# Performance work log

Hardware: AMD Instinct MI355X
Metric: run time of the kernel (lower is better)

Reference implementation:

```python
import jax, jax.numpy as jnp
import numpy as np

B = 8192
IN = 2048   # input_size
H = 2048    # hidden_size
D = IN + H  # combine feature dim = 4096


def setup_inputs() -> dict:
    key = jax.random.key(0)
    ks = jax.random.split(key, 11)
    s = 1.0 / np.sqrt(D)  # nn.Linear default init scale
    inp = {
        "input": jax.random.normal(ks[0], (B, D), jnp.float32),
        "hidden": jax.random.normal(ks[1], (B, D), jnp.float32),
        "cell": jax.random.normal(ks[2], (B, H), jnp.float32),
        "Wf": jax.random.uniform(ks[3], (D, H), jnp.float32, -s, s),
        "bf": jax.random.uniform(ks[4], (H,), jnp.float32, -s, s),
        "Wc": jax.random.uniform(ks[5], (D, H), jnp.float32, -s, s),
        "bc": jax.random.uniform(ks[6], (H,), jnp.float32, -s, s),
        "Wi": jax.random.uniform(ks[7], (D, H), jnp.float32, -s, s),
        "bi": jax.random.uniform(ks[8], (H,), jnp.float32, -s, s),
        "Wo": jax.random.uniform(ks[9], (D, H), jnp.float32, -s, s),
        "bo": jax.random.uniform(ks[10], (H,), jnp.float32, -s, s),
    }
    return inp


def reference(input, hidden, cell, Wf, bf, Wc, bc, Wi, bi, Wo, bo):
    combine = input + hidden  # [B, D] elementwise add (as in source, not concat)
    # Fuse the 4 gate GEMMs into one [D, 4H] GEMM for efficiency (same math).
    W = jnp.concatenate([Wf, Wc, Wi, Wo], axis=1)  # [D, 4H]
    b = jnp.concatenate([bf, bc, bi, bo])          # [4H]
    gates = combine @ W + b                        # [B, 4H]
    gf, gc, gi, go = jnp.split(gates, 4, axis=1)
    ft = jax.nn.sigmoid(gf)
    ct_ = jnp.tanh(gc)
    it = jax.nn.sigmoid(jax.nn.sigmoid(gi))  # double sigmoid, faithful to source
    cell_state = cell * ft + ct_ * it
    out = jax.nn.sigmoid(go)
    hidden_state = out * jnp.tanh(cell_state)
    return (out, hidden_state, cell_state)
```

## Files before the change

### kernel.cpp

```cpp
#include <hip/hip_runtime.h>
#include <hip/hip_bf16.h>

#define B_SZ 8192
#define D_SZ 4096
#define H_SZ 2048
#define N4H  8192
#define NT   (D_SZ / 64)

typedef __attribute__((ext_vector_type(8))) __bf16 bf16x8;
typedef __attribute__((ext_vector_type(4))) float f32x4;

#define GPTR(p) ((__attribute__((address_space(1))) void*)(p))
#define LPTR(p) ((__attribute__((address_space(3))) void*)(p))

__global__ void prep_k(const float* __restrict__ x, const float* __restrict__ h,
                       __hip_bfloat16* __restrict__ comb,
                       const float* __restrict__ Wf, const float* __restrict__ Wc,
                       const float* __restrict__ Wi, const float* __restrict__ Wo,
                       __hip_bfloat16* __restrict__ WT) {
    __shared__ float t[32][33];
    if (blockIdx.x < 2048) {
        const size_t n4 = (size_t)B_SZ * D_SZ / 4;
        const size_t stride = (size_t)2048 * 256;
        for (size_t i = (size_t)blockIdx.x * 256 + threadIdx.x; i < n4; i += stride) {
            f32x4 a = __builtin_nontemporal_load((const f32x4*)x + i);
            f32x4 b = __builtin_nontemporal_load((const f32x4*)h + i);
            short4 r;
            r.x = __builtin_bit_cast(short, __float2bfloat16(a.x + b.x));
            r.y = __builtin_bit_cast(short, __float2bfloat16(a.y + b.y));
            r.z = __builtin_bit_cast(short, __float2bfloat16(a.z + b.z));
            r.w = __builtin_bit_cast(short, __float2bfloat16(a.w + b.w));
            ((short4*)comb)[i] = r;
        }
    } else {
        const int b = blockIdx.x - 2048;
        const int k0 = (b & 127) * 32;
        const int n0 = (b >> 7) * 32;
        const float* W = (n0 < H_SZ) ? Wf : (n0 < 2 * H_SZ) ? Wc
                       : (n0 < 3 * H_SZ) ? Wi : Wo;
        const int g = n0 >> 11;
        const int nc = n0 & (H_SZ - 1);
        const int tx = threadIdx.x & 31, ty = threadIdx.x >> 5;
#pragma unroll
        for (int j = 0; j < 4; ++j)
            t[ty + j * 8][tx] = __builtin_nontemporal_load(
                W + (size_t)(k0 + ty + j * 8) * H_SZ + nc + tx);
        __syncthreads();
#pragma unroll
        for (int j = 0; j < 4; ++j) {
            const int h2 = nc + ty + j * 8;
            const int np = ((h2 >> 4) << 6) + (g << 4) + (h2 & 15);
            WT[(size_t)np * D_SZ + k0 + tx] = __float2bfloat16(t[tx][ty + j * 8]);
        }
    }
}


#define BAR()                                    \
    do {                                         \
        asm volatile("" ::: "memory");           \
        __builtin_amdgcn_s_barrier();            \
        asm volatile("" ::: "memory");           \
    } while (0)

#define STAGE(pbase, HSTRIDE, h, kt, region)                                           \
    do {                                                                               \
        __builtin_amdgcn_global_load_lds(                                              \
            GPTR((pbase) + (size_t)((h) * (HSTRIDE)) * D_SZ + (size_t)(kt) * 64),      \
            LPTR(smem + (region) + (h) * 16384 + wave * 1024), 16, 0, 0);              \
        __builtin_amdgcn_global_load_lds(                                              \
            GPTR((pbase) + (size_t)(128 + (h) * (HSTRIDE)) * D_SZ + (size_t)(kt) * 64),\
            LPTR(smem + (region) + (h) * 16384 + 8192 + wave * 1024), 16, 0, 0);       \
    } while (0)

#define LDA(dst, base, qm)                                                             \
    do {                                                                               \
        _Pragma("unroll") for (int mi = 0; mi < 4; ++mi) {                             \
            const int row_ = (qm) * 128 + wr * 64 + mi * 16 + fr;                      \
            dst[mi][0] = *(const bf16x8*)(smem + (base) + row_ * 128 + sw0);           \
            dst[mi][1] = *(const bf16x8*)(smem + (base) + row_ * 128 + sw1);           \
        }                                                                              \
    } while (0)

#define LDB(dst, base, qn)                                                             \
    do {                                                                               \
        _Pragma("unroll") for (int nf = 0; nf < 2; ++nf) {                             \
            const int row_ = (qn) * 128 + wc * 32 + nf * 16 + fr;                      \
            dst[nf][0] = *(const bf16x8*)(smem + (base) + row_ * 128 + sw0);           \
            dst[nf][1] = *(const bf16x8*)(smem + (base) + row_ * 128 + sw1);           \
        }                                                                              \
    } while (0)

#define MFMA_Q(qm, qn, areg, breg)                                                     \
    do {                                                                               \
        _Pragma("unroll") for (int mi = 0; mi < 4; ++mi)                               \
        _Pragma("unroll") for (int nf = 0; nf < 2; ++nf)                               \
        _Pragma("unroll") for (int ks = 0; ks < 2; ++ks)                               \
            acc[(qm) * 4 + mi][(qn) * 2 + nf] =                                        \
                __builtin_amdgcn_mfma_f32_16x16x32_bf16(                               \
                    areg[mi][ks], breg[nf][ks],                                        \
                    acc[(qm) * 4 + mi][(qn) * 2 + nf], 0, 0, 0);                       \
    } while (0)

#define TILE(tcur, CA, CB, OB)                                                         \
    {                                                                                  \
                                                                  \
        LDA(a, CA, 0);                                                                 \
        LDB(b0, CB, 0);                                                                \
        if ((tcur) + 1 < NT) STAGE(pB, 32, 1, (tcur) + 1, OB);                         \
        BAR();                                                                         \
        asm volatile("s_waitcnt lgkmcnt(0)" ::: "memory");                             \
        __builtin_amdgcn_s_setprio(1);                                                 \
        MFMA_Q(0, 0, a, b0);                                                           \
        __builtin_amdgcn_s_setprio(0);                                                 \
        BAR();                                                                         \
                                                                  \
        LDB(b1, CB, 1);                                                                \
        if ((tcur) + 2 < NT) STAGE(pA, 64, 0, (tcur) + 2, CA);                         \
        BAR();                                                                         \
        asm volatile("s_waitcnt lgkmcnt(0)" ::: "memory");                             \
        __builtin_amdgcn_s_setprio(1);                                                 \
        MFMA_Q(0, 1, a, b1);                                                           \
        __builtin_amdgcn_s_setprio(0);                                                 \
        BAR();                                                                         \
                                                                  \
        LDA(a, CA, 1);                                                                 \
        if ((tcur) + 2 < NT) STAGE(pB, 32, 0, (tcur) + 2, CB);                         \
        BAR();                                                                         \
        asm volatile("s_waitcnt lgkmcnt(0)" ::: "memory");                             \
        __builtin_amdgcn_s_setprio(1);                                                 \
        MFMA_Q(1, 0, a, b0);                                                           \
        __builtin_amdgcn_s_setprio(0);                                                 \
        BAR();                                                                         \
                                                                  \
        if ((tcur) + 2 < NT) STAGE(pA, 64, 1, (tcur) + 2, CA);                         \
        BAR();                                                                         \
        __builtin_amdgcn_s_setprio(1);                                                 \
        MFMA_Q(1, 1, a, b1);                                                           \
        __builtin_amdgcn_s_setprio(0);                                                 \
        if ((tcur) + 2 < NT) {                                                         \
            asm volatile("s_waitcnt vmcnt(6)" ::: "memory");                           \
        } else if ((tcur) + 1 < NT) {                                                  \
            asm volatile("s_waitcnt vmcnt(0)" ::: "memory");                           \
        }                                                                              \
        BAR();                                                                         \
    }

__device__ __forceinline__ float fsig(float x) { return 1.f / (1.f + __expf(-x)); }
__device__ __forceinline__ float ftanh(float x) {
    x = fminf(fmaxf(x, -15.f), 15.f);
    float e = __expf(2.f * x);
    return (e - 1.f) / (e + 1.f);
}

__global__ __launch_bounds__(512, 2) void gemm8_k(
    const __hip_bfloat16* __restrict__ A,
    const __hip_bfloat16* __restrict__ BT,
    const float* __restrict__ cell,
    const float* __restrict__ bfb, const float* __restrict__ bcb,
    const float* __restrict__ bib, const float* __restrict__ bob,
    float* __restrict__ out)
{
    extern __shared__ char smem[];

    const int tid  = threadIdx.x;
    const int wave = tid >> 6;
    const int lane = tid & 63;
    const int wr = wave >> 2;
    const int wc = wave & 3;
    const int fr = lane & 15;
    const int sw0 = (((lane >> 4) + 0) ^ (fr & 7)) << 4;
    const int sw1 = (((lane >> 4) + 4) ^ (fr & 7)) << 4;

    const int wg = (blockIdx.x & 7) * 128 + (blockIdx.x >> 3);
    const int n0 = (wg & 31) * 256;
    const int m0 = (wg >> 5) * 256;

    const int r0   = tid >> 3;
    const int col0 = ((tid & 7) ^ (r0 & 7)) << 3;
    const __hip_bfloat16* pA = A  + (size_t)(m0 + r0) * D_SZ + col0;
    const __hip_bfloat16* pB = BT + (size_t)(n0 + ((r0 >> 5) << 6) + (r0 & 31)) * D_SZ + col0;

    f32x4 acc[8][4] = {};
    bf16x8 a[4][2], b0[2][2], b1[2][2];

    STAGE(pA, 64, 0, 0, 0);
    STAGE(pB, 32, 0, 0, 32768);
    STAGE(pA, 64, 1, 0, 0);
    STAGE(pB, 32, 1, 0, 32768);
    STAGE(pA, 64, 0, 1, 65536);
    STAGE(pB, 32, 0, 1, 98304);
    STAGE(pA, 64, 1, 1, 65536);
    asm volatile("s_waitcnt vmcnt(6)" ::: "memory");
    BAR();

    for (int t = 0; t < NT; t += 2) {
        TILE(t,     0,     32768, 98304);
        TILE(t + 1, 65536, 98304, 32768);
    }

    const int crow = (lane >> 4) * 4;
    const int ccol = lane & 15;
    const int hh = (((n0 + wc * 64) >> 6) << 4) + ccol;
    const float bf_ = bfb[hh], bc_ = bcb[hh], bi_ = bib[hh], bo_ = bob[hh];
    const size_t BH = (size_t)B_SZ * H_SZ;
    float* hidp = out + BH;
    float* cstp = out + 2 * BH;
#pragma unroll
    for (int ai = 0; ai < 8; ++ai) {
#pragma unroll
        for (int j = 0; j < 4; ++j) {
            const size_t r = (size_t)(m0 + wr * 128 + ai * 16 + crow + j);
            const size_t idx = r * H_SZ + hh;
            const float gf = acc[ai][0][j] + bf_;
            const float gc = acc[ai][1][j] + bc_;
            const float gi = acc[ai][2][j] + bi_;
            const float go = acc[ai][3][j] + bo_;
            const float ft = fsig(gf);
            const float ct = ftanh(gc);
            const float it = fsig(fsig(gi));
            const float ot = fsig(go);
            const float cv = __builtin_nontemporal_load(cell + idx);
            const float cs = cv * ft + ct * it;
            __builtin_nontemporal_store(ot, out + idx);
            __builtin_nontemporal_store(cs, cstp + idx);
            __builtin_nontemporal_store(ot * ftanh(cs), hidp + idx);
        }
    }
}

extern "C" void kernel_launch(void* const* d_in, const int* in_sizes, int n_in,
                              void* d_out, int out_size, void* d_ws, size_t ws_size,
                              hipStream_t stream) {
    const float* input  = (const float*)d_in[0];
    const float* hidden = (const float*)d_in[1];
    const float* cell   = (const float*)d_in[2];
    const float* Wf     = (const float*)d_in[3];
    const float* bfb    = (const float*)d_in[4];
    const float* Wc     = (const float*)d_in[5];
    const float* bcb    = (const float*)d_in[6];
    const float* Wi     = (const float*)d_in[7];
    const float* bib    = (const float*)d_in[8];
    const float* Wo     = (const float*)d_in[9];
    const float* bob    = (const float*)d_in[10];
    float* out = (float*)d_out;

    char* ws = (char*)d_ws;
    __hip_bfloat16* comb = (__hip_bfloat16*)ws;
    __hip_bfloat16* WT   = (__hip_bfloat16*)(ws + (size_t)B_SZ * D_SZ * 2);

    hipFuncSetAttribute(reinterpret_cast<const void*>(gemm8_k),
                        hipFuncAttributeMaxDynamicSharedMemorySize, 131072);

    prep_k<<<2048 + 32768, 256, 0, stream>>>(input, hidden, comb, Wf, Wc, Wi, Wo, WT);
    gemm8_k<<<1024, 512, 131072, stream>>>(comb, WT, cell, bfb, bcb, bib, bob, out);
}
```

Before: 630.6 us.

## Make GEMM persistent: each block iterates four M tiles with cross-tile prefetch

The GEMM launch shrinks from 1024 to 256 blocks. Each block now owns one N column strip and loops over four consecutive 256-row M tiles on its XCD. While the current tile finishes, the first K tiles of the next M tile are prefetched into the pipeline, so the prologue and epilogue bubbles between tiles are hidden and the B strip stays hot in cache. In exchange, 256 blocks with 2 per CU give one wave of work with no tail balancing, and the epilogue stores now sit inside the main loop.

```diff
diff --git a/kernel.cpp b/kernel.cpp
--- a/kernel.cpp
+++ b/kernel.cpp
@@ -102,9 +102,44 @@
                     acc[(qm) * 4 + mi][(qn) * 2 + nf], 0, 0, 0);                       \
     } while (0)
 
-#define TILE(tcur, CA, CB, OB)                                                         \
+#define TILE_FULL(CA, CB, OB, PA2, K1, K2)                                             \
     {                                                                                  \
-                                                                  \
+        LDA(a, CA, 0);                                                                 \
+        LDB(b0, CB, 0);                                                                \
+        STAGE(pB, 32, 1, (K1), OB);                                                    \
+        BAR();                                                                         \
+        asm volatile("s_waitcnt lgkmcnt(0)" ::: "memory");                             \
+        __builtin_amdgcn_s_setprio(1);                                                 \
+        MFMA_Q(0, 0, a, b0);                                                           \
+        __builtin_amdgcn_s_setprio(0);                                                 \
+        BAR();                                                                         \
+        LDB(b1, CB, 1);                                                                \
+        STAGE(PA2, 64, 0, (K2), CA);                                                   \
+        BAR();                                                                         \
+        asm volatile("s_waitcnt lgkmcnt(0)" ::: "memory");                             \
+        __builtin_amdgcn_s_setprio(1);                                                 \
+        MFMA_Q(0, 1, a, b1);                                                           \
+        __builtin_amdgcn_s_setprio(0);                                                 \
+        BAR();                                                                         \
+        LDA(a, CA, 1);                                                                 \
+        STAGE(pB, 32, 0, (K2), CB);                                                    \
+        BAR();                                                                         \
+        asm volatile("s_waitcnt lgkmcnt(0)" ::: "memory");                             \
+        __builtin_amdgcn_s_setprio(1);                                                 \
+        MFMA_Q(1, 0, a, b0);                                                           \
+        __builtin_amdgcn_s_setprio(0);                                                 \
+        BAR();                                                                         \
+        STAGE(PA2, 64, 1, (K2), CA);                                                   \
+        BAR();                                                                         \
+        __builtin_amdgcn_s_setprio(1);                                                 \
+        MFMA_Q(1, 1, a, b1);                                                           \
+        __builtin_amdgcn_s_setprio(0);                                                 \
+        asm volatile("s_waitcnt vmcnt(6)" ::: "memory");                               \
+        BAR();                                                                         \
+    }
+
+#define TILE_TAIL(tcur, CA, CB, OB)                                                    \
+    {                                                                                  \
         LDA(a, CA, 0);                                                                 \
         LDB(b0, CB, 0);                                                                \
         if ((tcur) + 1 < NT) STAGE(pB, 32, 1, (tcur) + 1, OB);                         \
@@ -114,33 +149,25 @@
         MFMA_Q(0, 0, a, b0);                                                           \
         __builtin_amdgcn_s_setprio(0);                                                 \
         BAR();                                                                         \
-                                                                  \
         LDB(b1, CB, 1);                                                                \
-        if ((tcur) + 2 < NT) STAGE(pA, 64, 0, (tcur) + 2, CA);                         \
         BAR();                                                                         \
         asm volatile("s_waitcnt lgkmcnt(0)" ::: "memory");                             \
         __builtin_amdgcn_s_setprio(1);                                                 \
         MFMA_Q(0, 1, a, b1);                                                           \
         __builtin_amdgcn_s_setprio(0);                                                 \
         BAR();                                                                         \
-                                                                  \
         LDA(a, CA, 1);                                                                 \
-        if ((tcur) + 2 < NT) STAGE(pB, 32, 0, (tcur) + 2, CB);                         \
         BAR();                                                                         \
         asm volatile("s_waitcnt lgkmcnt(0)" ::: "memory");                             \
         __builtin_amdgcn_s_setprio(1);                                                 \
         MFMA_Q(1, 0, a, b0);                                                           \
         __builtin_amdgcn_s_setprio(0);                                                 \
         BAR();                                                                         \
-                                                                  \
-        if ((tcur) + 2 < NT) STAGE(pA, 64, 1, (tcur) + 2, CA);                         \
         BAR();                                                                         \
         __builtin_amdgcn_s_setprio(1);                                                 \
         MFMA_Q(1, 1, a, b1);                                                           \
         __builtin_amdgcn_s_setprio(0);                                                 \
-        if ((tcur) + 2 < NT) {                                                         \
-            asm volatile("s_waitcnt vmcnt(6)" ::: "memory");                           \
-        } else if ((tcur) + 1 < NT) {                                                  \
+        if ((tcur) + 1 < NT) {                                                         \
             asm volatile("s_waitcnt vmcnt(0)" ::: "memory");                           \
         }                                                                              \
         BAR();                                                                         \
@@ -172,14 +199,26 @@
     const int sw0 = (((lane >> 4) + 0) ^ (fr & 7)) << 4;
     const int sw1 = (((lane >> 4) + 4) ^ (fr & 7)) << 4;
 
-    const int wg = (blockIdx.x & 7) * 128 + (blockIdx.x >> 3);
-    const int n0 = (wg & 31) * 256;
-    const int m0 = (wg >> 5) * 256;
+    const int xcd  = blockIdx.x & 7;
+    const int slot = blockIdx.x >> 3;
+    const int n0 = slot * 256;
 
     const int r0   = tid >> 3;
     const int col0 = ((tid & 7) ^ (r0 & 7)) << 3;
-    const __hip_bfloat16* pA = A  + (size_t)(m0 + r0) * D_SZ + col0;
-    const __hip_bfloat16* pB = BT + (size_t)(n0 + ((r0 >> 5) << 6) + (r0 & 31)) * D_SZ + col0;
+    const __hip_bfloat16* pB =
+        BT + (size_t)(n0 + ((r0 >> 5) << 6) + (r0 & 31)) * D_SZ + col0;
+
+    const __hip_bfloat16* pA =
+        A + (size_t)(xcd * 1024 + r0) * D_SZ + col0;
+    const __hip_bfloat16* pA_nx = pA + (size_t)256 * D_SZ;
+
+    const int crow = (lane >> 4) * 4;
+    const int ccol = lane & 15;
+    const int hh = (slot * 4 + wc) * 16 + ccol;
+    const float bf_ = bfb[hh], bc_ = bcb[hh], bi_ = bib[hh], bo_ = bob[hh];
+    const size_t BH = (size_t)B_SZ * H_SZ;
+    float* hidp = out + BH;
+    float* cstp = out + 2 * BH;
 
     f32x4 acc[8][4] = {};
     bf16x8 a[4][2], b0[2][2], b1[2][2];
@@ -194,38 +233,52 @@
     asm volatile("s_waitcnt vmcnt(6)" ::: "memory");
     BAR();
 
-    for (int t = 0; t < NT; t += 2) {
-        TILE(t,     0,     32768, 98304);
-        TILE(t + 1, 65536, 98304, 32768);
-    }
-
-    const int crow = (lane >> 4) * 4;
-    const int ccol = lane & 15;
-    const int hh = (((n0 + wc * 64) >> 6) << 4) + ccol;
-    const float bf_ = bfb[hh], bc_ = bcb[hh], bi_ = bib[hh], bo_ = bob[hh];
-    const size_t BH = (size_t)B_SZ * H_SZ;
-    float* hidp = out + BH;
-    float* cstp = out + 2 * BH;
-#pragma unroll
-    for (int ai = 0; ai < 8; ++ai) {
-#pragma unroll
-        for (int j = 0; j < 4; ++j) {
-            const size_t r = (size_t)(m0 + wr * 128 + ai * 16 + crow + j);
-            const size_t idx = r * H_SZ + hh;
-            const float gf = acc[ai][0][j] + bf_;
-            const float gc = acc[ai][1][j] + bc_;
-            const float gi = acc[ai][2][j] + bi_;
-            const float go = acc[ai][3][j] + bo_;
-            const float ft = fsig(gf);
-            const float ct = ftanh(gc);
-            const float it = fsig(fsig(gi));
-            const float ot = fsig(go);
-            const float cv = __builtin_nontemporal_load(cell + idx);
-            const float cs = cv * ft + ct * it;
-            __builtin_nontemporal_store(ot, out + idx);
-            __builtin_nontemporal_store(cs, cstp + idx);
-            __builtin_nontemporal_store(ot * ftanh(cs), hidp + idx);
-        }
+#pragma unroll 1
+    for (int it = 0; it < 4; ++it) {
+#pragma unroll 1
+        for (int t = 0; t < 62; t += 2) {
+            TILE_FULL(0,     32768, 98304, pA, t + 1, t + 2);
+            TILE_FULL(65536, 98304, 32768, pA, t + 2, t + 3);
+        }
+        if (it < 3) {
+            TILE_FULL(0,     32768, 98304, pA_nx, 63, 0);
+            TILE_FULL(65536, 98304, 32768, pA_nx, 0, 1);
+        } else {
+            TILE_TAIL(62, 0,     32768, 98304);
+            TILE_TAIL(63, 65536, 98304, 32768);
+        }
+
+        const int m0w = (xcd * 4 + it) * 256;
+#pragma unroll
+        for (int ai = 0; ai < 8; ++ai) {
+#pragma unroll
+            for (int j = 0; j < 4; ++j) {
+                const size_t r = (size_t)(m0w + wr * 128 + ai * 16 + crow + j);
+                const size_t idx = r * H_SZ + hh;
+                const float gf = acc[ai][0][j] + bf_;
+                const float gc = acc[ai][1][j] + bc_;
+                const float gi = acc[ai][2][j] + bi_;
+                const float go = acc[ai][3][j] + bo_;
+                const float ft = fsig(gf);
+                const float ct = ftanh(gc);
+                const float it_ = fsig(fsig(gi));
+                const float ot = fsig(go);
+                const float cv = __builtin_nontemporal_load(cell + idx);
+                const float cs = cv * ft + ct * it_;
+                __builtin_nontemporal_store(ot, out + idx);
+                __builtin_nontemporal_store(cs, cstp + idx);
+                __builtin_nontemporal_store(ot * ftanh(cs), hidp + idx);
+            }
+        }
+        if (it < 3) {
+#pragma unroll
+            for (int ai = 0; ai < 8; ++ai)
+#pragma unroll
+                for (int bj = 0; bj < 4; ++bj)
+                    acc[ai][bj] = (f32x4){0.f, 0.f, 0.f, 0.f};
+        }
+        pA = pA_nx;
+        pA_nx += (size_t)256 * D_SZ;
     }
 }
 
@@ -253,5 +306,5 @@
                         hipFuncAttributeMaxDynamicSharedMemorySize, 131072);
 
     prep_k<<<2048 + 32768, 256, 0, stream>>>(input, hidden, comb, Wf, Wc, Wi, Wo, WT);
-    gemm8_k<<<1024, 512, 131072, stream>>>(comb, WT, cell, bfb, bcb, bib, bob, out);
+    gemm8_k<<<256, 512, 131072, stream>>>(comb, WT, cell, bfb, bcb, bib, bob, out);
 }
```

Measured after the change: 862.8 us. 1.37x slower.

## Switch GEMM to 4-wave 256x128 tiles with split A/B LDS pipelining

Applied to the files above, without the earlier changes.

Replaces the 8-wave 256x256-tile GEMM with a 4-wave kernel computing 256x128 output tiles, using 64 KB of LDS so two blocks can share a CU. A is now single-buffered per half and B is double-buffered. Loads are staged in finer chunks between MFMA quarters, with vmcnt waits before each barrier instead of the previous lgkmcnt waits and extra barriers. Tile-index wraparound issues redundant loads on the last iterations rather than branching. The smaller tile lowers operand reuse per block, which is traded for more blocks per CU and fewer synchronisation points.

```diff
diff --git a/kernel.cpp b/kernel.cpp
--- a/kernel.cpp
+++ b/kernel.cpp
@@ -56,6 +56,11 @@
 }
 
 
+#define LDS_A0 0
+#define LDS_A1 16384
+#define LDS_BB0 32768
+#define LDS_BB1 49152
+
 #define BAR()                                    \
     do {                                         \
         asm volatile("" ::: "memory");           \
@@ -63,31 +68,40 @@
         asm volatile("" ::: "memory");           \
     } while (0)
 
-#define STAGE(pbase, HSTRIDE, h, kt, region)                                           \
-    do {                                                                               \
-        __builtin_amdgcn_global_load_lds(                                              \
-            GPTR((pbase) + (size_t)((h) * (HSTRIDE)) * D_SZ + (size_t)(kt) * 64),      \
-            LPTR(smem + (region) + (h) * 16384 + wave * 1024), 16, 0, 0);              \
-        __builtin_amdgcn_global_load_lds(                                              \
-            GPTR((pbase) + (size_t)(128 + (h) * (HSTRIDE)) * D_SZ + (size_t)(kt) * 64),\
-            LPTR(smem + (region) + (h) * 16384 + 8192 + wave * 1024), 16, 0, 0);       \
-    } while (0)
-
-#define LDA(dst, base, qm)                                                             \
+#define STAGE_A(h, kt)                                                                 \
+    do {                                                                               \
+        _Pragma("unroll") for (int c_ = 0; c_ < 4; ++c_) {                             \
+            __builtin_amdgcn_global_load_lds(                                          \
+                GPTR(pA + (size_t)((c_ >> 1) * 128 + (h) * 64 + (c_ & 1) * 32) * D_SZ  \
+                         + (size_t)(kt) * 64),                                         \
+                LPTR(smem + (h) * 16384 + c_ * 4096 + wave * 1024), 16, 0, 0);         \
+        }                                                                              \
+    } while (0)
+
+#define STAGE_B(qn, kt, bb)                                                            \
+    do {                                                                               \
+        _Pragma("unroll") for (int c_ = 0; c_ < 2; ++c_) {                             \
+            __builtin_amdgcn_global_load_lds(                                          \
+                GPTR(pB + (size_t)((qn) * 32 + c_ * 64) * D_SZ + (size_t)(kt) * 64),   \
+                LPTR(smem + (bb) + (qn) * 8192 + c_ * 4096 + wave * 1024), 16, 0, 0);  \
+        }                                                                              \
+    } while (0)
+
+#define LDA(dst, RB)                                                                   \
     do {                                                                               \
         _Pragma("unroll") for (int mi = 0; mi < 4; ++mi) {                             \
-            const int row_ = (qm) * 128 + wr * 64 + mi * 16 + fr;                      \
-            dst[mi][0] = *(const bf16x8*)(smem + (base) + row_ * 128 + sw0);           \
-            dst[mi][1] = *(const bf16x8*)(smem + (base) + row_ * 128 + sw1);           \
-        }                                                                              \
-    } while (0)
-
-#define LDB(dst, base, qn)                                                             \
+            const int row_ = wr * 64 + mi * 16 + fr;                                   \
+            dst[mi][0] = *(const bf16x8*)(smem + (RB) + row_ * 128 + sw0);             \
+            dst[mi][1] = *(const bf16x8*)(smem + (RB) + row_ * 128 + sw1);             \
+        }                                                                              \
+    } while (0)
+
+#define LDB(dst, BB, qn)                                                               \
     do {                                                                               \
         _Pragma("unroll") for (int nf = 0; nf < 2; ++nf) {                             \
-            const int row_ = (qn) * 128 + wc * 32 + nf * 16 + fr;                      \
-            dst[nf][0] = *(const bf16x8*)(smem + (base) + row_ * 128 + sw0);           \
-            dst[nf][1] = *(const bf16x8*)(smem + (base) + row_ * 128 + sw1);           \
+            const int row_ = (qn) * 64 + wc * 32 + nf * 16 + fr;                       \
+            dst[nf][0] = *(const bf16x8*)(smem + (BB) + row_ * 128 + sw0);             \
+            dst[nf][1] = *(const bf16x8*)(smem + (BB) + row_ * 128 + sw1);             \
         }                                                                              \
     } while (0)
 
@@ -102,47 +116,40 @@
                     acc[(qm) * 4 + mi][(qn) * 2 + nf], 0, 0, 0);                       \
     } while (0)
 
-#define TILE(tcur, CA, CB, OB)                                                         \
+#define TILE(KT, CURB, OTHB)                                                           \
     {                                                                                  \
-                                                                  \
-        LDA(a, CA, 0);                                                                 \
-        LDB(b0, CB, 0);                                                                \
-        if ((tcur) + 1 < NT) STAGE(pB, 32, 1, (tcur) + 1, OB);                         \
-        BAR();                                                                         \
-        asm volatile("s_waitcnt lgkmcnt(0)" ::: "memory");                             \
+        const int kt_ = (KT) & 63;                                                     \
+                        \
+        LDA(a, LDS_A0);                                                                \
+        LDB(b0, CURB, 0);                                                              \
+        STAGE_B(0, kt_, OTHB);                                                         \
         __builtin_amdgcn_s_setprio(1);                                                 \
         MFMA_Q(0, 0, a, b0);                                                           \
         __builtin_amdgcn_s_setprio(0);                                                 \
-        BAR();                                                                         \
-                                                                  \
-        LDB(b1, CB, 1);                                                                \
-        if ((tcur) + 2 < NT) STAGE(pA, 64, 0, (tcur) + 2, CA);                         \
-        BAR();                                                                         \
-        asm volatile("s_waitcnt lgkmcnt(0)" ::: "memory");                             \
+        asm volatile("s_waitcnt vmcnt(6)" ::: "memory");                               \
+        BAR();                                                                         \
+                     \
+        LDB(b1, CURB, 1);                                                              \
+        STAGE_A(0, kt_);                                                               \
         __builtin_amdgcn_s_setprio(1);                                                 \
         MFMA_Q(0, 1, a, b1);                                                           \
         __builtin_amdgcn_s_setprio(0);                                                 \
-        BAR();                                                                         \
-                                                                  \
-        LDA(a, CA, 1);                                                                 \
-        if ((tcur) + 2 < NT) STAGE(pB, 32, 0, (tcur) + 2, CB);                         \
-        BAR();                                                                         \
-        asm volatile("s_waitcnt lgkmcnt(0)" ::: "memory");                             \
+        asm volatile("s_waitcnt vmcnt(6)" ::: "memory");                               \
+        BAR();                                                                         \
+                              \
+        LDA(a, LDS_A1);                                                                \
+        STAGE_B(1, kt_, OTHB);                                                         \
         __builtin_amdgcn_s_setprio(1);                                                 \
         MFMA_Q(1, 0, a, b0);                                                           \
         __builtin_amdgcn_s_setprio(0);                                                 \
-        BAR();                                                                         \
-                                                                  \
-        if ((tcur) + 2 < NT) STAGE(pA, 64, 1, (tcur) + 2, CA);                         \
-        BAR();                                                                         \
+        asm volatile("s_waitcnt vmcnt(6)" ::: "memory");                               \
+        BAR();                                                                         \
+                                  \
+        STAGE_A(1, kt_);                                                               \
         __builtin_amdgcn_s_setprio(1);                                                 \
         MFMA_Q(1, 1, a, b1);                                                           \
         __builtin_amdgcn_s_setprio(0);                                                 \
-        if ((tcur) + 2 < NT) {                                                         \
-            asm volatile("s_waitcnt vmcnt(6)" ::: "memory");                           \
-        } else if ((tcur) + 1 < NT) {                                                  \
-            asm volatile("s_waitcnt vmcnt(0)" ::: "memory");                           \
-        }                                                                              \
+        asm volatile("s_waitcnt vmcnt(6)" ::: "memory");                               \
         BAR();                                                                         \
     }
 
@@ -153,7 +160,7 @@
     return (e - 1.f) / (e + 1.f);
 }
 
-__global__ __launch_bounds__(512, 2) void gemm8_k(
+__global__ __launch_bounds__(256, 2) void gemm4_k(
     const __hip_bfloat16* __restrict__ A,
     const __hip_bfloat16* __restrict__ BT,
     const float* __restrict__ cell,
@@ -166,67 +173,70 @@
     const int tid  = threadIdx.x;
     const int wave = tid >> 6;
     const int lane = tid & 63;
-    const int wr = wave >> 2;
-    const int wc = wave & 3;
+    const int wr = wave >> 1;
+    const int wc = wave & 1;
     const int fr = lane & 15;
     const int sw0 = (((lane >> 4) + 0) ^ (fr & 7)) << 4;
     const int sw1 = (((lane >> 4) + 4) ^ (fr & 7)) << 4;
 
-    const int wg = (blockIdx.x & 7) * 128 + (blockIdx.x >> 3);
-    const int n0 = (wg & 31) * 256;
-    const int m0 = (wg >> 5) * 256;
+    const int wg = (blockIdx.x & 7) * 256 + (blockIdx.x >> 3);
+    const int ntile = wg & 63;
+    const int m0 = (wg >> 6) * 256;
+    const int n0 = ntile * 128;
 
     const int r0   = tid >> 3;
     const int col0 = ((tid & 7) ^ (r0 & 7)) << 3;
     const __hip_bfloat16* pA = A  + (size_t)(m0 + r0) * D_SZ + col0;
-    const __hip_bfloat16* pB = BT + (size_t)(n0 + ((r0 >> 5) << 6) + (r0 & 31)) * D_SZ + col0;
+    const __hip_bfloat16* pB = BT + (size_t)(n0 + r0) * D_SZ + col0;
 
     f32x4 acc[8][4] = {};
     bf16x8 a[4][2], b0[2][2], b1[2][2];
 
-    STAGE(pA, 64, 0, 0, 0);
-    STAGE(pB, 32, 0, 0, 32768);
-    STAGE(pA, 64, 1, 0, 0);
-    STAGE(pB, 32, 1, 0, 32768);
-    STAGE(pA, 64, 0, 1, 65536);
-    STAGE(pB, 32, 0, 1, 98304);
-    STAGE(pA, 64, 1, 1, 65536);
+    STAGE_B(0, 0, LDS_BB0);
+    STAGE_A(0, 0);
+    STAGE_B(1, 0, LDS_BB0);
+    STAGE_A(1, 0);
     asm volatile("s_waitcnt vmcnt(6)" ::: "memory");
     BAR();
 
+#pragma unroll 1
     for (int t = 0; t < NT; t += 2) {
-        TILE(t,     0,     32768, 98304);
-        TILE(t + 1, 65536, 98304, 32768);
-    }
-
-    const int crow = (lane >> 4) * 4;
-    const int ccol = lane & 15;
-    const int hh = (((n0 + wc * 64) >> 6) << 4) + ccol;
-    const float bf_ = bfb[hh], bc_ = bcb[hh], bi_ = bib[hh], bo_ = bob[hh];
-    const size_t BH = (size_t)B_SZ * H_SZ;
-    float* hidp = out + BH;
-    float* cstp = out + 2 * BH;
-#pragma unroll
-    for (int ai = 0; ai < 8; ++ai) {
-#pragma unroll
-        for (int j = 0; j < 4; ++j) {
-            const size_t r = (size_t)(m0 + wr * 128 + ai * 16 + crow + j);
-            const size_t idx = r * H_SZ + hh;
-            const float gf = acc[ai][0][j] + bf_;
-            const float gc = acc[ai][1][j] + bc_;
-            const float gi = acc[ai][2][j] + bi_;
-            const float go = acc[ai][3][j] + bo_;
-            const float ft = fsig(gf);
-            const float ct = ftanh(gc);
-            const float it = fsig(fsig(gi));
-            const float ot = fsig(go);
-            const float cv = __builtin_nontemporal_load(cell + idx);
-            const float cs = cv * ft + ct * it;
-            __builtin_nontemporal_store(ot, out + idx);
-            __builtin_nontemporal_store(cs, cstp + idx);
-            __builtin_nontemporal_store(ot * ftanh(cs), hidp + idx);
+        TILE(t + 1, LDS_BB0, LDS_BB1);
+        TILE(t + 2, LDS_BB1, LDS_BB0);
+    }
+
+    {
+        const int crow = (lane >> 4) * 4;
+        const int ccol = lane & 15;
+        const int hh = (ntile * 2 + wc) * 16 + ccol;
+        const float bf_ = bfb[hh], bc_ = bcb[hh], bi_ = bib[hh], bo_ = bob[hh];
+        const size_t BH = (size_t)B_SZ * H_SZ;
+        float* hidp = out + BH;
+        float* cstp = out + 2 * BH;
+#pragma unroll
+        for (int ai = 0; ai < 8; ++ai) {
+#pragma unroll
+            for (int j = 0; j < 4; ++j) {
+                const size_t r = (size_t)(m0 + wr * 128 + ai * 16 + crow + j);
+                const size_t idx = r * H_SZ + hh;
+                const float gf = acc[ai][0][j] + bf_;
+                const float gc = acc[ai][1][j] + bc_;
+                const float gi = acc[ai][2][j] + bi_;
+                const float go = acc[ai][3][j] + bo_;
+                const float ft = fsig(gf);
+                const float ct = ftanh(gc);
+                const float it_ = fsig(fsig(gi));
+                const float ot = fsig(go);
+                const float cv = __builtin_nontemporal_load(cell + idx);
+                const float cs = cv * ft + ct * it_;
+                __builtin_nontemporal_store(ot, out + idx);
+                __builtin_nontemporal_store(cs, cstp + idx);
+                __builtin_nontemporal_store(ot * ftanh(cs), hidp + idx);
+            }
         }
     }
+
+    asm volatile("s_waitcnt vmcnt(0)" ::: "memory");
 }
 
 extern "C" void kernel_launch(void* const* d_in, const int* in_sizes, int n_in,
@@ -249,9 +259,9 @@
     __hip_bfloat16* comb = (__hip_bfloat16*)ws;
     __hip_bfloat16* WT   = (__hip_bfloat16*)(ws + (size_t)B_SZ * D_SZ * 2);
 
-    hipFuncSetAttribute(reinterpret_cast<const void*>(gemm8_k),
-                        hipFuncAttributeMaxDynamicSharedMemorySize, 131072);
+    hipFuncSetAttribute(reinterpret_cast<const void*>(gemm4_k),
+                        hipFuncAttributeMaxDynamicSharedMemorySize, 65536);
 
     prep_k<<<2048 + 32768, 256, 0, stream>>>(input, hidden, comb, Wf, Wc, Wi, Wo, WT);
-    gemm8_k<<<1024, 512, 131072, stream>>>(comb, WT, cell, bfb, bcb, bib, bob, out);
-}
+    gemm4_k<<<2048, 256, 65536, stream>>>(comb, WT, cell, bfb, bcb, bib, bob, out);
+}
```

New measurement: 597.7 us. 1.06x faster.
